# Performance work log

Hardware: AMD Instinct MI355X
Metric: run time of the kernel (lower is better)

## Reference

```python
import jax, jax.numpy as jnp
import numpy as np

B, T, FEATS, HEAD = 2, 2048, 2048, 16
DIM_HEAD = FEATS // HEAD
EPS = float(jnp.finfo(jnp.float32).eps)  # torch nn.RMSNorm default eps=None -> dtype eps


def _rms_norm(u, g):
    # u: [..., d]; torch RMSNorm: u / sqrt(mean(u^2) + eps) * g
    return u * jax.lax.rsqrt(jnp.mean(u * u, axis=-1, keepdims=True) + EPS) * g


def setup_inputs() -> dict:
    key = jax.random.key(0)
    kx, kw = jax.random.split(key)
    x = jax.random.normal(kx, (B, T, FEATS), dtype=jnp.float32)
    W = jax.random.normal(kw, (FEATS, FEATS), dtype=jnp.float32) / np.sqrt(FEATS)
    g1 = jnp.ones((DIM_HEAD,), dtype=jnp.float32)
    g2 = jnp.ones((DIM_HEAD,), dtype=jnp.float32)
    g3 = jnp.ones((DIM_HEAD,), dtype=jnp.float32)
    return {"x": x, "W": W, "g1": g1, "g2": g2, "g3": g3}


def reference(x, W, g1, g2, g3):
    Bb, Tt, C = x.shape
    sqrt_d = jnp.asarray(DIM_HEAD ** 0.5, dtype=x.dtype)
    # tied QKV projection: torch Linear -> x @ W.T ; then split heads -> [B,H,T,D]
    w = (x @ W.T).reshape(Bb, Tt, HEAD, DIM_HEAD).transpose(0, 2, 1, 3)
    q = _rms_norm(w, g1)
    k = _rms_norm(w, g2)
    v = _rms_norm(w, g3)
    att = jnp.einsum("bhid,bhjd->bhij", q, k) / sqrt_d  # [B,H,T,T]
    # symmetric row + column softmax
    score = jax.nn.softmax(att, axis=-1) + jax.nn.softmax(att, axis=-2)
    y = jnp.einsum("bhij,bhjd->bihd", score, v).reshape(Bb, Tt, C)
    # F.linear(y, W.t()) == y @ W  (tied-weight reprojection)
    return y @ W
```

## Files before the change

kernel.cpp:

```cpp
#include <hip/hip_runtime.h>
#include <stdint.h>

#define T_SEQ 2048
#define B_SZ 2
#define N_HEAD 16
#define D_HEAD 128
#define C_DIM 2048
#define M_ROWS (B_SZ*T_SEQ)
#define N_BH (B_SZ*N_HEAD)

typedef _Float16 f16;
typedef f16 f16x8 __attribute__((ext_vector_type(8)));
typedef f16 f16x4 __attribute__((ext_vector_type(4)));
typedef float f32x4 __attribute__((ext_vector_type(4)));

#define MFMA_F16(a,b,c) __builtin_amdgcn_mfma_f32_16x16x32_f16(a,b,c,0,0,0)

#define BAR_LGKM() do { asm volatile("s_waitcnt lgkmcnt(0)" ::: "memory"); \
                        __builtin_amdgcn_s_barrier(); } while (0)
#define BAR_ALL()  do { asm volatile("s_waitcnt vmcnt(0) lgkmcnt(0)" ::: "memory"); \
                        __builtin_amdgcn_s_barrier(); } while (0)

__device__ __forceinline__ float fexp2(float x) {
#if __has_builtin(__builtin_amdgcn_exp2f)
  return __builtin_amdgcn_exp2f(x);
#else
  float r; asm("v_exp_f32 %0, %1" : "=v"(r) : "v"(x)); return r;
#endif
}

__device__ __forceinline__ void gl_lds16(const void* g, void* l) {
  __builtin_amdgcn_global_load_lds(
      (const __attribute__((address_space(1))) unsigned int*)g,
      (__attribute__((address_space(3))) unsigned int*)l, 16, 0, 0);
}

#define MB_SCALE 0.12752924444069595f
#define RMS_EPS  1.1920928955078125e-07f

__global__ void k_prep_w(const float* __restrict__ W, f16* __restrict__ Wb,
                         f16* __restrict__ Wtb) {
  __shared__ float tile[64][65];
  const int bx = blockIdx.x * 64;
  const int by = blockIdx.y * 64;
  const int t = threadIdx.x;
  const int tc = t & 63, tr4 = t >> 6;
  for (int rr = tr4; rr < 64; rr += 4) {
    float v = W[(size_t)(by + rr) * C_DIM + bx + tc];
    tile[rr][tc] = v;
    Wb[(size_t)(by + rr) * C_DIM + bx + tc] = (f16)v;
  }
  __syncthreads();
  for (int rr = tr4; rr < 64; rr += 4) {
    Wtb[(size_t)(bx + rr) * C_DIM + by + tc] = (f16)tile[tc][rr];
  }
}

__global__ void k_prep_x(const float* __restrict__ x, f16* __restrict__ xb) {
  int i = blockIdx.x * blockDim.x + threadIdx.x;
  const int stride = gridDim.x * blockDim.x;
  const int n4 = (M_ROWS * C_DIM) / 4;
  for (; i < n4; i += stride) {
    f32x4 v = ((const f32x4*)x)[i];
    f16x4 o; o[0]=(f16)v[0]; o[1]=(f16)v[1]; o[2]=(f16)v[2]; o[3]=(f16)v[3];
    ((f16x4*)xb)[i] = o;
  }
}

template<typename OT>
__global__ __launch_bounds__(256, 2)
void k_gemm_bt(const f16* __restrict__ A, const f16* __restrict__ Bm,
               OT* __restrict__ C, int Nd, int Kd) {
  __shared__ __align__(16) f16 As[2][128 * 64];
  __shared__ __align__(16) f16 Bs[2][128 * 64];
  const int tid = threadIdx.x;
  const int lane = tid & 63, wid = tid >> 6;
  const int lr = lane & 15, lkg = lane >> 4;
  const int wr = wid >> 1, wc = wid & 1;
  const int tm = blockIdx.y * 128, tn = blockIdx.x * 128;

  f32x4 acc[4][4];
#pragma unroll
  for (int i = 0; i < 4; ++i)
#pragma unroll
    for (int j = 0; j < 4; ++j) acc[i][j] = (f32x4){0.f, 0.f, 0.f, 0.f};

  const int nkt = Kd >> 6;

  auto stage = [&](int buf, int kt) {
    const int k0 = kt << 6;
    for (int s = 0; s < 4; ++s) {
      const int r0 = (wid * 4 + s) * 8;
      const int r = r0 + (lane >> 3);
      const int lg = ((lane & 7) ^ (r & 7)) << 3;
      gl_lds16(A + (size_t)(tm + r) * Kd + k0 + lg, &As[buf][r0 * 64]);
      gl_lds16(Bm + (size_t)(tn + r) * Kd + k0 + lg, &Bs[buf][r0 * 64]);
    }
  };

  stage(0, 0);
  int cur = 0;
  for (int kt = 0; kt < nkt; ++kt) {
    __syncthreads();
    if (kt + 1 < nkt) stage(cur ^ 1, kt + 1);
#pragma unroll
    for (int kk = 0; kk < 2; ++kk) {
      f16x8 a[4], b[4];
#pragma unroll
      for (int i = 0; i < 4; ++i) {
        const int ra = wr * 64 + i * 16 + lr;
        const int ga = ((kk * 4 + lkg) ^ (ra & 7)) << 3;
        a[i] = *(const f16x8*)&As[cur][ra * 64 + ga];
        const int rb = wc * 64 + i * 16 + lr;
        const int gb = ((kk * 4 + lkg) ^ (rb & 7)) << 3;
        b[i] = *(const f16x8*)&Bs[cur][rb * 64 + gb];
      }
#pragma unroll
      for (int i = 0; i < 4; ++i)
#pragma unroll
        for (int j = 0; j < 4; ++j) acc[i][j] = MFMA_F16(a[i], b[j], acc[i][j]);
    }
    cur ^= 1;
  }
#pragma unroll
  for (int i = 0; i < 4; ++i) {
    const int row0 = tm + wr * 64 + i * 16 + lkg * 4;
#pragma unroll
    for (int j = 0; j < 4; ++j) {
      const int col = tn + wc * 64 + j * 16 + lr;
#pragma unroll
      for (int r = 0; r < 4; ++r)
        C[(size_t)(row0 + r) * Nd + col] = (OT)acc[i][j][r];
    }
  }
}

__global__ __launch_bounds__(256, 2)
void k_gemm_qkv(const f16* __restrict__ A, const f16* __restrict__ Bm,
                const float* __restrict__ g1, const float* __restrict__ g2,
                f16* __restrict__ nb, f16* __restrict__ mb,
                f16* __restrict__ nT) {
  __shared__ __align__(16) char smem[70656];
  f16 (*As)[128 * 64] = (f16(*)[128 * 64])smem;
  f16 (*Bs)[128 * 64] = (f16(*)[128 * 64])(smem + 32768);
  f16* Cs = (f16*)smem;
  float* sc = (float*)(smem + 69632);

  const int tid = threadIdx.x;
  const int lane = tid & 63, wid = tid >> 6;
  const int lr = lane & 15, lkg = lane >> 4;
  const int wr = wid >> 1, wc = wid & 1;
  const int tm = blockIdx.y * 128;
  const int hh = blockIdx.x;
  const int tn = hh * 128;

  f32x4 acc[4][4];
#pragma unroll
  for (int i = 0; i < 4; ++i)
#pragma unroll
    for (int j = 0; j < 4; ++j) acc[i][j] = (f32x4){0.f, 0.f, 0.f, 0.f};

  auto stage = [&](int buf, int kt) {
    const int k0 = kt << 6;
    for (int s = 0; s < 4; ++s) {
      const int r0 = (wid * 4 + s) * 8;
      const int r = r0 + (lane >> 3);
      const int lg = ((lane & 7) ^ (r & 7)) << 3;
      gl_lds16(A + (size_t)(tm + r) * C_DIM + k0 + lg, &As[buf][r0 * 64]);
      gl_lds16(Bm + (size_t)(tn + r) * C_DIM + k0 + lg, &Bs[buf][r0 * 64]);
    }
  };

  stage(0, 0);
  int cur = 0;
  for (int kt = 0; kt < 32; ++kt) {
    __syncthreads();
    if (kt + 1 < 32) stage(cur ^ 1, kt + 1);
#pragma unroll
    for (int kk = 0; kk < 2; ++kk) {
      f16x8 a[4], b[4];
#pragma unroll
      for (int i = 0; i < 4; ++i) {
        const int ra = wr * 64 + i * 16 + lr;
        const int ga = ((kk * 4 + lkg) ^ (ra & 7)) << 3;
        a[i] = *(const f16x8*)&As[cur][ra * 64 + ga];
        const int rb = wc * 64 + i * 16 + lr;
        const int gb = ((kk * 4 + lkg) ^ (rb & 7)) << 3;
        b[i] = *(const f16x8*)&Bs[cur][rb * 64 + gb];
      }
#pragma unroll
      for (int i = 0; i < 4; ++i)
#pragma unroll
        for (int j = 0; j < 4; ++j) acc[i][j] = MFMA_F16(a[i], b[j], acc[i][j]);
    }
    cur ^= 1;
  }
  __syncthreads();

#pragma unroll
  for (int i = 0; i < 4; ++i)
#pragma unroll
    for (int j = 0; j < 4; ++j)
#pragma unroll
      for (int r = 0; r < 4; ++r)
        Cs[(wr * 64 + i * 16 + lkg * 4 + r) * 136 + wc * 64 + j * 16 + lr] =
            (f16)acc[i][j][r];
  __syncthreads();

  const int row = tid >> 1, dh = tid & 1;
  f16x8 v[8];
  float ss = 0.f;
#pragma unroll
  for (int c = 0; c < 8; ++c) {
    v[c] = *(const f16x8*)&Cs[row * 136 + dh * 64 + c * 8];
#pragma unroll
    for (int e = 0; e < 8; ++e) { float f = (float)v[c][e]; ss += f * f; }
  }
  ss += __shfl_xor(ss, 1);
  const float scale = rsqrtf(ss * (1.f / 128.f) + RMS_EPS);
  if (dh == 0) sc[row] = scale;

  const int grow = tm + row;
  const int b = grow >> 11, ts = grow & (T_SEQ - 1);
  const size_t nbase =
      ((size_t)((b * N_HEAD + hh) * T_SEQ + ts)) * 128 + dh * 64;
#pragma unroll
  for (int c = 0; c < 8; ++c) {
    const int d0 = dh * 64 + c * 8;
    f16x8 n8, m8;
#pragma unroll
    for (int e = 0; e < 8; ++e) {
      const float nf = (float)v[c][e] * scale;
      n8[e] = (f16)nf;
      m8[e] = (f16)(nf * g1[d0 + e] * g2[d0 + e] * MB_SCALE);
    }
    *(f16x8*)&nb[nbase + c * 8] = n8;
    *(f16x8*)&mb[nbase + c * 8] = m8;
  }
  __syncthreads();

  const int dcol = tid >> 1, th = tid & 1;
  const size_t tbase =
      ((size_t)((b * N_HEAD + hh) * 128 + dcol)) * T_SEQ + (tm & (T_SEQ - 1)) +
      th * 64;
#pragma unroll
  for (int rr = 0; rr < 8; ++rr) {
    f16x8 o;
#pragma unroll
    for (int e = 0; e < 8; ++e) {
      const int trow = th * 64 + rr * 8 + e;
      o[e] = (f16)((float)Cs[trow * 136 + dcol] * sc[trow]);
    }
    *(f16x8*)&nT[tbase + rr * 8] = o;
  }
}

__global__ __launch_bounds__(256, 2)
void k_stats(const f16* __restrict__ mIn, const f16* __restrict__ nIn,
             float* __restrict__ alpha) {
  __shared__ __align__(16) f16 Ns[2][128 * 128];
  __shared__ float red[256];
  const int tid = threadIdx.x, lane = tid & 63, wid = tid >> 6;
  const int lr = lane & 15, lkg = lane >> 4;
  const int wr = wid >> 1, wc = wid & 1;
  const int lin = blockIdx.x + (blockIdx.y << 4);
  const int swz = ((lin & 7) << 6) + (lin >> 3);
  const int it = swz & 15, bh = swz >> 4;
  const f16* mp = mIn + (size_t)bh * T_SEQ * 128;
  const f16* np = nIn + (size_t)bh * T_SEQ * 128;

  f16x8 msr[4][4];
#pragma unroll
  for (int i = 0; i < 4; ++i)
#pragma unroll
    for (int kk = 0; kk < 4; ++kk)
      msr[i][kk] = *(const f16x8*)&mp[(size_t)(it * 128 + wr * 64 + i * 16 + lr) * 128 +
                                      (kk * 4 + lkg) * 8];

  auto stageN = [&](int buf, int jt) {
#pragma unroll
    for (int s = 0; s < 8; ++s) {
      const int r0 = (wid * 8 + s) * 4;
      const int r = r0 + (lane >> 4);
      const int lg = ((lane & 15) ^ (r & 7)) << 3;
      gl_lds16(np + (size_t)(jt * 128 + r) * 128 + lg, &Ns[buf][r0 * 128]);
    }
  };

  float srun[16];
#pragma unroll
  for (int q = 0; q < 16; ++q) srun[q] = 0.f;

  stageN(0, 0);
  BAR_ALL();
  int cur = 0;
  for (int jt = 0; jt < 16; ++jt) {
    if (jt < 15) stageN(cur ^ 1, jt + 1);
    f32x4 acc[4][4];
#pragma unroll
    for (int i = 0; i < 4; ++i)
#pragma unroll
      for (int j = 0; j < 4; ++j) acc[i][j] = (f32x4){0.f, 0.f, 0.f, 0.f};
#pragma unroll
    for (int kk = 0; kk < 4; ++kk) {
      f16x8 b[4];
#pragma unroll
      for (int j = 0; j < 4; ++j) {
        const int rb = wc * 64 + j * 16 + lr;
        const int gb = ((kk * 4 + lkg) ^ (rb & 7)) << 3;
        b[j] = *(const f16x8*)&Ns[cur][rb * 128 + gb];
      }
#pragma unroll
      for (int i = 0; i < 4; ++i)
#pragma unroll
        for (int j = 0; j < 4; ++j)
          acc[i][j] = MFMA_F16(msr[i][kk], b[j], acc[i][j]);
    }
#pragma unroll
    for (int i = 0; i < 4; ++i)
#pragma unroll
      for (int r = 0; r < 4; ++r) {
        float s = fexp2(acc[i][0][r]) + fexp2(acc[i][1][r]) +
                  fexp2(acc[i][2][r]) + fexp2(acc[i][3][r]);
        srun[i * 4 + r] += s;
      }
    BAR_ALL();
    cur ^= 1;
  }
#pragma unroll
  for (int q = 0; q < 16; ++q) {
    float v = srun[q];
    v += __shfl_xor(v, 1); v += __shfl_xor(v, 2);
    v += __shfl_xor(v, 4); v += __shfl_xor(v, 8);
    srun[q] = v;
  }
  if (lr == 0) {
#pragma unroll
    for (int q = 0; q < 16; ++q) {
      const int row = wr * 64 + (q >> 2) * 16 + lkg * 4 + (q & 3);
      red[row * 2 + wc] = srun[q];
    }
  }
  __syncthreads();
  if (tid < 128) {
    const float s = red[tid * 2] + red[tid * 2 + 1];
    alpha[(size_t)bh * T_SEQ + it * 128 + tid] = 1.f / s;
  }
}

__global__ __launch_bounds__(256, 2)
void k_apply(const f16* __restrict__ mIn, const f16* __restrict__ nIn,
             const f16* __restrict__ nTIn, const float* __restrict__ alpha,
             const float* __restrict__ g3, f16* __restrict__ yb) {
  __shared__ __align__(16) f16 Ns[2][64 * 128];
  __shared__ __align__(16) f16 Nts[2][128 * 64];
  __shared__ __align__(16) f16 Ps[128 * 64];
  const int tid = threadIdx.x, lane = tid & 63, wid = tid >> 6;
  const int lr = lane & 15, lkg = lane >> 4;
  const int wj = wid >> 1;
  const int wi = wid & 1;
  const int lin = blockIdx.x + (blockIdx.y << 4);
  const int swz = ((lin & 7) << 6) + (lin >> 3);
  const int it = swz & 15, bh = swz >> 4;
  const int b = bh >> 4, hh = bh & 15;
  const f16* mp = mIn + (size_t)bh * T_SEQ * 128;
  const f16* np = nIn + (size_t)bh * T_SEQ * 128;
  const f16* ntp = nTIn + (size_t)bh * 128 * T_SEQ;
  const float* al = alpha + (size_t)bh * T_SEQ;

  f16x8 msr[4][4];
#pragma unroll
  for (int ii = 0; ii < 4; ++ii)
#pragma unroll
    for (int kk = 0; kk < 4; ++kk)
      msr[ii][kk] = *(const f16x8*)&mp[(size_t)(it * 128 + wi * 64 + ii * 16 + lr) * 128 +
                                       (kk * 4 + lkg) * 8];

  auto stageN = [&](int buf, int jt) {
#pragma unroll
    for (int s = 0; s < 4; ++s) {
      const int r0 = (wid * 4 + s) * 4;
      const int r = r0 + (lane >> 4);
      const int lg = ((lane & 15) ^ (r & 7)) << 3;
      gl_lds16(np + (size_t)(jt * 64 + r) * 128 + lg, &Ns[buf][r0 * 128]);
    }
  };
  auto stageNT = [&](int buf, int jt) {
#pragma unroll
    for (int s = 0; s < 4; ++s) {
      const int r0 = (wid * 4 + s) * 8;
      const int r = r0 + (lane >> 3);
      const int lg = ((lane & 7) ^ (r & 7)) << 3;
      gl_lds16(ntp + (size_t)r * T_SEQ + jt * 64 + lg, &Nts[buf][r0 * 64]);
    }
  };

  float ai[4];
#pragma unroll
  for (int ii = 0; ii < 4; ++ii) ai[ii] = al[it * 128 + wi * 64 + ii * 16 + lr];

  f32x4 yacc[4][4];
#pragma unroll
  for (int i = 0; i < 4; ++i)
#pragma unroll
    for (int j = 0; j < 4; ++j) yacc[i][j] = (f32x4){0.f, 0.f, 0.f, 0.f};

  stageN(0, 0);
  stageNT(0, 0);
  BAR_ALL();
  int cur = 0;
  for (int jt = 0; jt < 32; ++jt) {
    float aj[8];
#pragma unroll
    for (int jj = 0; jj < 2; ++jj)
#pragma unroll
      for (int r = 0; r < 4; ++r)
        aj[jj * 4 + r] = al[jt * 64 + wj * 32 + jj * 16 + lkg * 4 + r];
    if (jt < 31) { stageN(cur ^ 1, jt + 1); stageNT(cur ^ 1, jt + 1); }

    f32x4 acc[2][4];
#pragma unroll
    for (int i = 0; i < 2; ++i)
#pragma unroll
      for (int j = 0; j < 4; ++j) acc[i][j] = (f32x4){0.f, 0.f, 0.f, 0.f};
#pragma unroll
    for (int kk = 0; kk < 4; ++kk) {
      f16x8 a[2];
#pragma unroll
      for (int jj = 0; jj < 2; ++jj) {
        const int jrow = wj * 32 + jj * 16 + lr;
        a[jj] = *(const f16x8*)&Ns[cur][jrow * 128 + (((kk * 4 + lkg) ^ (jrow & 7)) << 3)];
      }
#pragma unroll
      for (int jj = 0; jj < 2; ++jj)
#pragma unroll
        for (int ii = 0; ii < 4; ++ii)
          acc[jj][ii] = MFMA_F16(a[jj], msr[ii][kk], acc[jj][ii]);
    }

#pragma unroll
    for (int jj = 0; jj < 2; ++jj)
#pragma unroll
      for (int ii = 0; ii < 4; ++ii) {
        f16x4 o;
#pragma unroll
        for (int r = 0; r < 4; ++r) {
          const float p = fexp2(acc[jj][ii][r]) * (ai[ii] + aj[jj * 4 + r]);
          o[r] = (f16)p;
        }
        const int il = wi * 64 + ii * 16 + lr;
        const int jl = wj * 32 + jj * 16 + lkg * 4;
        *(f16x4*)&Ps[il * 64 + (((jl >> 3) ^ (il & 7)) << 3) + (jl & 7)] = o;
      }
    BAR_LGKM();

#pragma unroll
    for (int kk = 0; kk < 2; ++kk) {
      f16x8 a[4], bfr[4];
#pragma unroll
      for (int dd = 0; dd < 4; ++dd) {
        const int drow = wj * 64 + dd * 16 + lr;
        a[dd] = *(const f16x8*)&Nts[cur][drow * 64 + (((kk * 4 + lkg) ^ (drow & 7)) << 3)];
      }
#pragma unroll
      for (int ii = 0; ii < 4; ++ii) {
        const int irow = wi * 64 + ii * 16 + lr;
        bfr[ii] = *(const f16x8*)&Ps[irow * 64 + (((kk * 4 + lkg) ^ (irow & 7)) << 3)];
      }
#pragma unroll
      for (int dd = 0; dd < 4; ++dd)
#pragma unroll
        for (int ii = 0; ii < 4; ++ii)
          yacc[dd][ii] = MFMA_F16(a[dd], bfr[ii], yacc[dd][ii]);
    }
    BAR_ALL();
    cur ^= 1;
  }

#pragma unroll
  for (int dd = 0; dd < 4; ++dd) {
    const int d0 = wj * 64 + dd * 16 + lkg * 4;
    float g3v[4];
#pragma unroll
    for (int r = 0; r < 4; ++r) g3v[r] = g3[d0 + r];
#pragma unroll
    for (int ii = 0; ii < 4; ++ii) {
      const int icol = wi * 64 + ii * 16 + lr;
      const size_t base =
          ((size_t)(b * T_SEQ + it * 128 + icol)) * C_DIM + hh * 128 + d0;
      f16x4 o;
#pragma unroll
      for (int r = 0; r < 4; ++r) o[r] = (f16)(yacc[dd][ii][r] * g3v[r]);
      *(f16x4*)&yb[base] = o;
    }
  }
}

extern "C" void kernel_launch(void* const* d_in, const int* in_sizes, int n_in,
                              void* d_out, int out_size, void* d_ws,
                              size_t ws_size, hipStream_t stream) {
  const float* x = (const float*)d_in[0];
  const float* W = (const float*)d_in[1];
  const float* g1 = (const float*)d_in[2];
  const float* g2 = (const float*)d_in[3];
  const float* g3 = (const float*)d_in[4];
  float* out = (float*)d_out;
  char* ws = (char*)d_ws;

  f16* xb   = (f16*)(ws);
  f16* Wb   = (f16*)(ws + 16777216);
  f16* Wtb  = (f16*)(ws + 25165824);
  f16* nb   = (f16*)(ws + 50331648);
  f16* mb   = (f16*)(ws + 67108864);
  f16* nT   = (f16*)(ws + 83886080);
  f16* yb   = (f16*)(ws + 100663296);
  float* alpha = (float*)(ws + 117440512);

  k_prep_w<<<dim3(32, 32), 256, 0, stream>>>(W, Wb, Wtb);
  k_prep_x<<<dim3(2048), 256, 0, stream>>>(x, xb);
  k_gemm_qkv<<<dim3(16, 32), 256, 0, stream>>>(xb, Wb, g1, g2, nb, mb, nT);
  k_stats<<<dim3(16, 32), 256, 0, stream>>>(mb, nb, alpha);
  k_apply<<<dim3(16, 32), 256, 0, stream>>>(mb, nb, nT, alpha, g3, yb);
  k_gemm_bt<float><<<dim3(16, 32), 256, 0, stream>>>(yb, Wtb, out, C_DIM, C_DIM);
}
```

Measured before the change: 227.9 us.

## Exploit score symmetry in stats pass and fuse prep kernels

Because q and k are the same normalized tensor, the score matrix is symmetric. The stats pass now computes only upper-triangular 128x128 tiles and atomically adds both row sums and column sums into a zeroed buffer, then a small kernel inverts them into alpha. This roughly halves the QK MFMA and exp work in the stats pass, at the cost of a memset, atomics and an extra launch. The W transpose/convert and x convert kernels are also merged into one launch.

```diff
diff --git a/kernel.cpp b/kernel.cpp
--- a/kernel.cpp
+++ b/kernel.cpp
@@ -38,32 +38,34 @@
 #define MB_SCALE 0.12752924444069595f
 #define RMS_EPS  1.1920928955078125e-07f
 
-__global__ void k_prep_w(const float* __restrict__ W, f16* __restrict__ Wb,
-                         f16* __restrict__ Wtb) {
+__global__ void k_prep(const float* __restrict__ W, const float* __restrict__ x,
+                       f16* __restrict__ Wb, f16* __restrict__ Wtb,
+                       f16* __restrict__ xb) {
   __shared__ float tile[64][65];
-  const int bx = blockIdx.x * 64;
-  const int by = blockIdx.y * 64;
+  const int lin = blockIdx.x;
   const int t = threadIdx.x;
-  const int tc = t & 63, tr4 = t >> 6;
-  for (int rr = tr4; rr < 64; rr += 4) {
-    float v = W[(size_t)(by + rr) * C_DIM + bx + tc];
-    tile[rr][tc] = v;
-    Wb[(size_t)(by + rr) * C_DIM + bx + tc] = (f16)v;
-  }
-  __syncthreads();
-  for (int rr = tr4; rr < 64; rr += 4) {
-    Wtb[(size_t)(bx + rr) * C_DIM + by + tc] = (f16)tile[tc][rr];
-  }
-}
-
-__global__ void k_prep_x(const float* __restrict__ x, f16* __restrict__ xb) {
-  int i = blockIdx.x * blockDim.x + threadIdx.x;
-  const int stride = gridDim.x * blockDim.x;
-  const int n4 = (M_ROWS * C_DIM) / 4;
-  for (; i < n4; i += stride) {
-    f32x4 v = ((const f32x4*)x)[i];
-    f16x4 o; o[0]=(f16)v[0]; o[1]=(f16)v[1]; o[2]=(f16)v[2]; o[3]=(f16)v[3];
-    ((f16x4*)xb)[i] = o;
+  if (lin < 1024) {
+    const int bx = (lin & 31) * 64;
+    const int by = (lin >> 5) * 64;
+    const int tc = t & 63, tr4 = t >> 6;
+    for (int rr = tr4; rr < 64; rr += 4) {
+      float v = W[(size_t)(by + rr) * C_DIM + bx + tc];
+      tile[rr][tc] = v;
+      Wb[(size_t)(by + rr) * C_DIM + bx + tc] = (f16)v;
+    }
+    __syncthreads();
+    for (int rr = tr4; rr < 64; rr += 4) {
+      Wtb[(size_t)(bx + rr) * C_DIM + by + tc] = (f16)tile[tc][rr];
+    }
+  } else {
+    int i = (lin - 1024) * 256 + t;
+    const int stride = 2048 * 256;
+    const int n4 = (M_ROWS * C_DIM) / 4;
+    for (; i < n4; i += stride) {
+      f32x4 v = ((const f32x4*)x)[i];
+      f16x4 o; o[0]=(f16)v[0]; o[1]=(f16)v[1]; o[2]=(f16)v[2]; o[3]=(f16)v[3];
+      ((f16x4*)xb)[i] = o;
+    }
   }
 }
 
@@ -255,17 +257,19 @@
   }
 }
 
-__global__ __launch_bounds__(256, 2)
-void k_stats(const f16* __restrict__ mIn, const f16* __restrict__ nIn,
-             float* __restrict__ alpha) {
-  __shared__ __align__(16) f16 Ns[2][128 * 128];
-  __shared__ float red[256];
+__global__ __launch_bounds__(256, 3)
+void k_stats_tri(const f16* __restrict__ mIn, const f16* __restrict__ nIn,
+                 float* __restrict__ Ssum) {
+  __shared__ __align__(16) f16 Ns[128 * 128];
+  __shared__ float redR[256];
+  __shared__ float redC[256];
   const int tid = threadIdx.x, lane = tid & 63, wid = tid >> 6;
   const int lr = lane & 15, lkg = lane >> 4;
   const int wr = wid >> 1, wc = wid & 1;
-  const int lin = blockIdx.x + (blockIdx.y << 4);
-  const int swz = ((lin & 7) << 6) + (lin >> 3);
-  const int it = swz & 15, bh = swz >> 4;
+  int p = blockIdx.x, it = 0, rowlen = 16;
+  while (p >= rowlen) { p -= rowlen; ++it; --rowlen; }
+  const int jt = it + p;
+  const int bh = blockIdx.y;
   const f16* mp = mIn + (size_t)bh * T_SEQ * 128;
   const f16* np = nIn + (size_t)bh * T_SEQ * 128;
 
@@ -277,75 +281,96 @@
       msr[i][kk] = *(const f16x8*)&mp[(size_t)(it * 128 + wr * 64 + i * 16 + lr) * 128 +
                                       (kk * 4 + lkg) * 8];
 
-  auto stageN = [&](int buf, int jt) {
-#pragma unroll
-    for (int s = 0; s < 8; ++s) {
-      const int r0 = (wid * 8 + s) * 4;
-      const int r = r0 + (lane >> 4);
-      const int lg = ((lane & 15) ^ (r & 7)) << 3;
-      gl_lds16(np + (size_t)(jt * 128 + r) * 128 + lg, &Ns[buf][r0 * 128]);
-    }
-  };
-
-  float srun[16];
-#pragma unroll
-  for (int q = 0; q < 16; ++q) srun[q] = 0.f;
-
-  stageN(0, 0);
+#pragma unroll
+  for (int s = 0; s < 8; ++s) {
+    const int r0 = (wid * 8 + s) * 4;
+    const int r = r0 + (lane >> 4);
+    const int lg = ((lane & 15) ^ (r & 7)) << 3;
+    gl_lds16(np + (size_t)(jt * 128 + r) * 128 + lg, &Ns[r0 * 128]);
+  }
   BAR_ALL();
-  int cur = 0;
-  for (int jt = 0; jt < 16; ++jt) {
-    if (jt < 15) stageN(cur ^ 1, jt + 1);
-    f32x4 acc[4][4];
+
+  f32x4 acc[4][4];
+#pragma unroll
+  for (int i = 0; i < 4; ++i)
+#pragma unroll
+    for (int j = 0; j < 4; ++j) acc[i][j] = (f32x4){0.f, 0.f, 0.f, 0.f};
+#pragma unroll
+  for (int kk = 0; kk < 4; ++kk) {
+    f16x8 b[4];
+#pragma unroll
+    for (int j = 0; j < 4; ++j) {
+      const int rb = wc * 64 + j * 16 + lr;
+      const int gb = ((kk * 4 + lkg) ^ (rb & 7)) << 3;
+      b[j] = *(const f16x8*)&Ns[rb * 128 + gb];
+    }
 #pragma unroll
     for (int i = 0; i < 4; ++i)
 #pragma unroll
-      for (int j = 0; j < 4; ++j) acc[i][j] = (f32x4){0.f, 0.f, 0.f, 0.f};
-#pragma unroll
-    for (int kk = 0; kk < 4; ++kk) {
-      f16x8 b[4];
-#pragma unroll
-      for (int j = 0; j < 4; ++j) {
-        const int rb = wc * 64 + j * 16 + lr;
-        const int gb = ((kk * 4 + lkg) ^ (rb & 7)) << 3;
-        b[j] = *(const f16x8*)&Ns[cur][rb * 128 + gb];
-      }
-#pragma unroll
-      for (int i = 0; i < 4; ++i)
-#pragma unroll
-        for (int j = 0; j < 4; ++j)
-          acc[i][j] = MFMA_F16(msr[i][kk], b[j], acc[i][j]);
-    }
-#pragma unroll
-    for (int i = 0; i < 4; ++i)
+      for (int j = 0; j < 4; ++j)
+        acc[i][j] = MFMA_F16(msr[i][kk], b[j], acc[i][j]);
+  }
+
+  float rsum[16], csum[4];
+#pragma unroll
+  for (int q = 0; q < 16; ++q) rsum[q] = 0.f;
+#pragma unroll
+  for (int j = 0; j < 4; ++j) csum[j] = 0.f;
+#pragma unroll
+  for (int i = 0; i < 4; ++i)
+#pragma unroll
+    for (int j = 0; j < 4; ++j)
 #pragma unroll
       for (int r = 0; r < 4; ++r) {
-        float s = fexp2(acc[i][0][r]) + fexp2(acc[i][1][r]) +
-                  fexp2(acc[i][2][r]) + fexp2(acc[i][3][r]);
-        srun[i * 4 + r] += s;
-      }
-    BAR_ALL();
-    cur ^= 1;
-  }
+        const float e = fexp2(acc[i][j][r]);
+        rsum[i * 4 + r] += e;
+        csum[j] += e;
+      }
 #pragma unroll
   for (int q = 0; q < 16; ++q) {
-    float v = srun[q];
+    float v = rsum[q];
     v += __shfl_xor(v, 1); v += __shfl_xor(v, 2);
     v += __shfl_xor(v, 4); v += __shfl_xor(v, 8);
-    srun[q] = v;
+    rsum[q] = v;
   }
   if (lr == 0) {
 #pragma unroll
     for (int q = 0; q < 16; ++q) {
       const int row = wr * 64 + (q >> 2) * 16 + lkg * 4 + (q & 3);
-      red[row * 2 + wc] = srun[q];
+      redR[row * 2 + wc] = rsum[q];
+    }
+  }
+#pragma unroll
+  for (int j = 0; j < 4; ++j) {
+    float v = csum[j];
+    v += __shfl_xor(v, 16); v += __shfl_xor(v, 32);
+    csum[j] = v;
+  }
+  if (lkg == 0) {
+#pragma unroll
+    for (int j = 0; j < 4; ++j) {
+      const int col = wc * 64 + j * 16 + lr;
+      redC[col * 2 + wr] = csum[j];
     }
   }
   __syncthreads();
   if (tid < 128) {
-    const float s = red[tid * 2] + red[tid * 2 + 1];
-    alpha[(size_t)bh * T_SEQ + it * 128 + tid] = 1.f / s;
-  }
+    const float rS = redR[tid * 2] + redR[tid * 2 + 1];
+    atomicAdd(&Ssum[(size_t)bh * T_SEQ + it * 128 + tid], rS);
+    if (it != jt) {
+      const float cS = redC[tid * 2] + redC[tid * 2 + 1];
+      atomicAdd(&Ssum[(size_t)bh * T_SEQ + jt * 128 + tid], cS);
+    }
+  }
+}
+
+__global__ void k_inv(const float* __restrict__ S, float* __restrict__ alpha) {
+  const int i = blockIdx.x * blockDim.x + threadIdx.x;
+  f32x4 s = ((const f32x4*)S)[i];
+  f32x4 a;
+#pragma unroll
+  for (int e = 0; e < 4; ++e) a[e] = 1.f / s[e];
+  ((f32x4*)alpha)[i] = a;
 }
 
 __global__ __launch_bounds__(256, 2)
@@ -515,11 +540,13 @@
   f16* nT   = (f16*)(ws + 83886080);
   f16* yb   = (f16*)(ws + 100663296);
   float* alpha = (float*)(ws + 117440512);
-
-  k_prep_w<<<dim3(32, 32), 256, 0, stream>>>(W, Wb, Wtb);
-  k_prep_x<<<dim3(2048), 256, 0, stream>>>(x, xb);
+  float* Ssum  = (float*)(ws + 117702656);
+
+  hipMemsetAsync(Ssum, 0, 262144, stream);
+  k_prep<<<dim3(3072), 256, 0, stream>>>(W, x, Wb, Wtb, xb);
   k_gemm_qkv<<<dim3(16, 32), 256, 0, stream>>>(xb, Wb, g1, g2, nb, mb, nT);
-  k_stats<<<dim3(16, 32), 256, 0, stream>>>(mb, nb, alpha);
+  k_stats_tri<<<dim3(136, 32), 256, 0, stream>>>(mb, nb, Ssum);
+  k_inv<<<dim3(64), 256, 0, stream>>>(Ssum, alpha);
   k_apply<<<dim3(16, 32), 256, 0, stream>>>(mb, nb, nT, alpha, g3, yb);
   k_gemm_bt<float><<<dim3(16, 32), 256, 0, stream>>>(yb, Wtb, out, C_DIM, C_DIM);
 }
```

Measured after the change: 237.7 us. +4.3%, slower.
